# Performance work log

Measured on AMD Instinct MI355X. Metric: run time of the kernel, lower is better.

The kernel has to match this reference:

```python
import jax, jax.numpy as jnp
import numpy as np

BATCH, TIME, NUM_CLASSES = 128, 512, 1024
SAMPLE_OUT_SIZE = TIME          # input_length == sample_out_size == time
DUMMY_WORD = 2
EPS = 1e-8


def setup_inputs() -> dict:
    key = jax.random.key(0)
    # class probabilities (layer applies log(inputs + 1e-8) itself)
    inputs = jax.random.uniform(key, (BATCH, TIME, NUM_CLASSES), dtype=jnp.float32)
    return {"inputs": inputs}


def reference(inputs):
    """CTC greedy decode (merge_repeated=False) + sparse_to_dense(default=-1)
    + pad with dummy_word, sliced to sample_out_size. Returns [B, T] int32."""
    B, T, V = inputs.shape
    blank = V - 1  # TF CTC blank label = num_classes - 1

    logp = jnp.log(inputs + EPS)                       # faithful to layer
    ids = jnp.argmax(logp, axis=-1)                    # [B, T] greedy path

    nonblank = ids != blank                            # merge_repeated=False: only drop blanks
    counts = jnp.sum(nonblank, axis=1)                 # [B] decoded length per row
    max_len = jnp.max(counts)                          # dense_shape[1] of the SparseTensor

    # stable left-compaction of non-blank tokens (argsort is stable in jax)
    keys = jnp.where(nonblank, 0, 1).astype(jnp.int32)
    order = jnp.argsort(keys, axis=1)                  # [B, T]
    compacted = jnp.take_along_axis(ids, order, axis=1)  # [B, T]

    pos = jnp.arange(T)[None, :]                       # [1, T]
    # j <  counts[b]        -> decoded token
    # counts[b] <= j < L    -> -1   (sparse_to_dense default)
    # L <= j < T            -> dummy_word (concatenated dummy vector)
    out = jnp.where(
        pos < counts[:, None],
        compacted,
        jnp.where(pos < max_len, -1, DUMMY_WORD),
    ).astype(jnp.int32)
    return out
```

## Files before the change

### kernel.cpp

```cpp
#include <hip/hip_runtime.h>
#include <hip/hip_bf16.h>

#define BATCH 128
#define TIME 512
#define NUM_CLASSES 1024
#define BLANK (NUM_CLASSES - 1)
#define DUMMY_WORD 2

__global__ __launch_bounds__(256) void argmax_kernel(
    const float* __restrict__ in, int* __restrict__ ids) {
    int wid = blockIdx.x * 4 + (threadIdx.x >> 6);
    int lane = threadIdx.x & 63;
    const float4* p = (const float4*)(in + (size_t)wid * NUM_CLASSES);

    float best = -1.0f;
    int bidx = 0;
#pragma unroll
    for (int k = 0; k < 4; k++) {
        float4 v = p[lane + k * 64];
        int base = 4 * (lane + k * 64);
        if (v.x > best) { best = v.x; bidx = base; }
        if (v.y > best) { best = v.y; bidx = base + 1; }
        if (v.z > best) { best = v.z; bidx = base + 2; }
        if (v.w > best) { best = v.w; bidx = base + 3; }
    }
#pragma unroll
    for (int m = 32; m >= 1; m >>= 1) {
        float ov = __shfl_xor(best, m, 64);
        int   oi = __shfl_xor(bidx, m, 64);
        if (ov > best || (ov == best && oi < bidx)) { best = ov; bidx = oi; }
    }
    if (lane == 0) ids[wid] = bidx;
}

__global__ __launch_bounds__(64) void compact_kernel(
    int* __restrict__ ids, int* __restrict__ counts) {
    int b = blockIdx.x;
    int lane = threadIdx.x;
    int* row = ids + b * TIME;

    const int4* r4 = (const int4*)row;
    int4 a = r4[lane * 2];
    int4 c = r4[lane * 2 + 1];
    int vals[8] = {a.x, a.y, a.z, a.w, c.x, c.y, c.z, c.w};

    int cnt = 0;
#pragma unroll
    for (int j = 0; j < 8; j++) cnt += (vals[j] != BLANK);

    int incl = cnt;
#pragma unroll
    for (int off = 1; off < 64; off <<= 1) {
        int n = __shfl_up(incl, off, 64);
        if (lane >= off) incl += n;
    }
    int pos = incl - cnt;
#pragma unroll
    for (int j = 0; j < 8; j++) {
        if (vals[j] != BLANK) { row[pos] = vals[j]; pos++; }
    }
    if (lane == 63) counts[b] = incl;
}

__global__ __launch_bounds__(512) void finalize_kernel(
    const int* __restrict__ counts, int* __restrict__ out) {
    __shared__ int smem[BATCH];
    __shared__ int s_max;
    int b = blockIdx.x;
    int t = threadIdx.x;
    if (t < BATCH) smem[t] = counts[t];
    __syncthreads();
    if (t == 0) {
        int m = 0;
        for (int i = 0; i < BATCH; i++) m = max(m, smem[i]);
        s_max = m;
    }
    __syncthreads();
    int cnt = smem[b];
    if (t >= cnt) out[b * TIME + t] = (t < s_max) ? -1 : DUMMY_WORD;
}

extern "C" void kernel_launch(void* const* d_in, const int* in_sizes, int n_in,
                              void* d_out, int out_size, void* d_ws, size_t ws_size,
                              hipStream_t stream) {
    const float* in = (const float*)d_in[0];
    int* out = (int*)d_out;
    int* counts = (int*)d_ws;

    argmax_kernel<<<(BATCH * TIME) / 4, 256, 0, stream>>>(in, out);
    compact_kernel<<<BATCH, 64, 0, stream>>>(out, counts);
    finalize_kernel<<<BATCH, 512, 0, stream>>>(counts, out);
}
```

Before: 350.1 us.

## Fuse compaction and finalize via per-block nonblank partial counts from argmax

The argmax kernel now collects each block's four ids in shared memory, writes them as one int4, and emits a per-block count of non-blank tokens. A single fused kernel then reduces these partials to get the global max length redundantly in every block, compacts its row, and fills the padding. This removes the separate finalize launch and its dependency on a counts buffer. In exchange it adds a block barrier in argmax and redundant partial reads in every compaction block.

```diff
diff --git a/kernel.cpp b/kernel.cpp
--- a/kernel.cpp
+++ b/kernel.cpp
@@ -1,5 +1,4 @@
 #include <hip/hip_runtime.h>
-#include <hip/hip_bf16.h>
 
 #define BATCH 128
 #define TIME 512
@@ -8,8 +7,11 @@
 #define DUMMY_WORD 2
 
 __global__ __launch_bounds__(256) void argmax_kernel(
-    const float* __restrict__ in, int* __restrict__ ids) {
-    int wid = blockIdx.x * 4 + (threadIdx.x >> 6);
+    const float* __restrict__ in, int* __restrict__ ids,
+    int* __restrict__ partials) {
+    __shared__ int s_idx[4];
+    int wave = threadIdx.x >> 6;
+    int wid = blockIdx.x * 4 + wave;
     int lane = threadIdx.x & 63;
     const float4* p = (const float4*)(in + (size_t)wid * NUM_CLASSES);
 
@@ -30,15 +32,36 @@
         int   oi = __shfl_xor(bidx, m, 64);
         if (ov > best || (ov == best && oi < bidx)) { best = ov; bidx = oi; }
     }
-    if (lane == 0) ids[wid] = bidx;
+    if (lane == 0) s_idx[wave] = bidx;
+    __syncthreads();
+    if (threadIdx.x == 0) {
+        ((int4*)ids)[blockIdx.x] =
+            make_int4(s_idx[0], s_idx[1], s_idx[2], s_idx[3]);
+        partials[blockIdx.x] = (s_idx[0] != BLANK) + (s_idx[1] != BLANK) +
+                               (s_idx[2] != BLANK) + (s_idx[3] != BLANK);
+    }
 }
 
-__global__ __launch_bounds__(64) void compact_kernel(
-    int* __restrict__ ids, int* __restrict__ counts) {
+__global__ __launch_bounds__(64) void fused_kernel(
+    const int* __restrict__ partials, int* __restrict__ ids) {
     int b = blockIdx.x;
     int lane = threadIdx.x;
+
+    const int4* p4 = (const int4*)partials;
+    int ca = 0, cb = 0;
+#pragma unroll 4
+    for (int j = 0; j < 32; j++) {
+        int4 u = p4[lane * 32 + j];
+        ca += u.x + u.y + u.z + u.w;
+        int4 w = p4[(lane + 64) * 32 + j];
+        cb += w.x + w.y + w.z + w.w;
+    }
+    int ml = max(ca, cb);
+#pragma unroll
+    for (int m = 32; m >= 1; m >>= 1)
+        ml = max(ml, __shfl_xor(ml, m, 64));
+
     int* row = ids + b * TIME;
-
     const int4* r4 = (const int4*)row;
     int4 a = r4[lane * 2];
     int4 c = r4[lane * 2 + 1];
@@ -59,25 +82,10 @@
     for (int j = 0; j < 8; j++) {
         if (vals[j] != BLANK) { row[pos] = vals[j]; pos++; }
     }
-    if (lane == 63) counts[b] = incl;
-}
+    int total = __shfl(incl, 63, 64);
 
-__global__ __launch_bounds__(512) void finalize_kernel(
-    const int* __restrict__ counts, int* __restrict__ out) {
-    __shared__ int smem[BATCH];
-    __shared__ int s_max;
-    int b = blockIdx.x;
-    int t = threadIdx.x;
-    if (t < BATCH) smem[t] = counts[t];
-    __syncthreads();
-    if (t == 0) {
-        int m = 0;
-        for (int i = 0; i < BATCH; i++) m = max(m, smem[i]);
-        s_max = m;
-    }
-    __syncthreads();
-    int cnt = smem[b];
-    if (t >= cnt) out[b * TIME + t] = (t < s_max) ? -1 : DUMMY_WORD;
+    for (int t = total + lane; t < TIME; t += 64)
+        row[t] = (t < ml) ? -1 : DUMMY_WORD;
 }
 
 extern "C" void kernel_launch(void* const* d_in, const int* in_sizes, int n_in,
@@ -85,9 +93,8 @@
                               hipStream_t stream) {
     const float* in = (const float*)d_in[0];
     int* out = (int*)d_out;
-    int* counts = (int*)d_ws;
+    int* partials = (int*)d_ws;
 
-    argmax_kernel<<<(BATCH * TIME) / 4, 256, 0, stream>>>(in, out);
-    compact_kernel<<<BATCH, 64, 0, stream>>>(out, counts);
-    finalize_kernel<<<BATCH, 512, 0, stream>>>(counts, out);
+    argmax_kernel<<<(BATCH * TIME) / 4, 256, 0, stream>>>(in, out, partials);
+    fused_kernel<<<BATCH, 64, 0, stream>>>(partials, out);
 }
```

New measurement: 352.0 us. Within noise of the previous version (+0.5%).
